# Optimization experiments

Hardware: AMD Instinct MI355X
Metric: run time of the kernel (lower is better)

The kernel has to match this reference:

```python
import jax, jax.numpy as jnp
import numpy as np

B, T, S, D, H, DK = 2, 2048, 2048, 1024, 16, 64


def setup_inputs() -> dict:
    key = jax.random.key(0)
    ks = jax.random.split(key, 11)
    s = 1.0 / np.sqrt(D)
    return {
        "query": jax.random.normal(ks[0], (B, T, D), jnp.float32),
        "value": jax.random.normal(ks[1], (B, S, D), jnp.float32),
        "key": jax.random.normal(ks[2], (B, S, D), jnp.float32),
        "Wq": jax.random.normal(ks[3], (D, H, DK), jnp.float32) * s,
        "bq": jnp.zeros((H, DK), jnp.float32),
        "Wk": jax.random.normal(ks[4], (D, H, DK), jnp.float32) * s,
        "bk": jnp.zeros((H, DK), jnp.float32),
        "Wv": jax.random.normal(ks[5], (D, H, DK), jnp.float32) * s,
        "bv": jnp.zeros((H, DK), jnp.float32),
        "Wo": jax.random.normal(ks[6], (H, DK, D), jnp.float32) * (1.0 / np.sqrt(H * DK)),
        "bo": jnp.zeros((D,), jnp.float32),
    }


def reference(query, value, key, Wq, bq, Wk, bk, Wv, bv, Wo, bo):
    # Projections: (B, seq, D) x (D, H, DK) -> (B, seq, H, DK)
    q = jnp.einsum("btd,dhk->bthk", query, Wq) + bq
    k = jnp.einsum("bsd,dhk->bshk", key, Wk) + bk
    v = jnp.einsum("bsd,dhk->bshk", value, Wv) + bv
    # Scaled dot-product attention (keras scales query by 1/sqrt(key_dim))
    q = q * (1.0 / np.sqrt(DK)).astype(np.float32)
    scores = jnp.einsum("bshk,bthk->bhts", k, q)  # (B, H, T, S)
    probs = jax.nn.softmax(scores, axis=-1)
    attn = jnp.einsum("bhts,bshk->bthk", probs, v)  # (B, T, H, DK)
    # Output projection back to model dim
    out = jnp.einsum("bthk,hkd->btd", attn, Wo) + bo
    return out
```

## Files before the change

### kernel.cpp

```cpp
#include <hip/hip_runtime.h>
#include <math.h>

#define BB  2
#define TT  2048
#define SSQ 2048
#define DD  1024
#define HH  16
#define DKK 64
#define MM  (BB*TT)
#define NN  (HH*DKK)

typedef __attribute__((ext_vector_type(8))) short short8;
typedef __attribute__((ext_vector_type(4))) float f32x4;
typedef __attribute__((ext_vector_type(2))) unsigned int uint2v;
typedef __attribute__((ext_vector_type(4))) unsigned int u32x4;

__device__ __forceinline__ short f2bf(float x) {
    unsigned u = __builtin_bit_cast(unsigned, x);
    unsigned r = (u + 0x7FFFu + ((u >> 16) & 1u)) >> 16;
    return (short)r;
}

__device__ __forceinline__ unsigned pk2(float lo, float hi) {
    return (__builtin_bit_cast(unsigned, hi) & 0xFFFF0000u) |
           (__builtin_bit_cast(unsigned, lo) >> 16);
}

__device__ __forceinline__ void glds16(const void* g, void* l) {
    __builtin_amdgcn_global_load_lds(
        (const __attribute__((address_space(1))) void*)g,
        (__attribute__((address_space(3))) void*)l, 16, 0, 0);
}

__global__ __launch_bounds__(256)
void to_bf16_acts(const float* __restrict__ a0, const float* __restrict__ a1,
                  const float* __restrict__ a2,
                  short* __restrict__ o0, short* __restrict__ o1,
                  short* __restrict__ o2)
{
    int z = blockIdx.y;
    const float* in = (z == 0) ? a0 : (z == 1) ? a1 : a2;
    short* out = (z == 0) ? o0 : (z == 1) ? o1 : o2;
    size_t i0 = ((size_t)blockIdx.x * 256 + threadIdx.x) * 8;
    f32x4 f0 = *(const f32x4*)(in + i0);
    f32x4 f1 = *(const f32x4*)(in + i0 + 4);
    short8 v;
#pragma unroll
    for (int j = 0; j < 4; j++) v[j] = f2bf(f0[j]);
#pragma unroll
    for (int j = 0; j < 4; j++) v[4 + j] = f2bf(f1[j]);
    *(short8*)(out + i0) = v;
}

__global__ __launch_bounds__(256)
void wtrans(const float* __restrict__ w0, const float* __restrict__ w1,
            const float* __restrict__ w2, const float* __restrict__ w3,
            short* __restrict__ t0, short* __restrict__ t1,
            short* __restrict__ t2, short* __restrict__ t3)
{
    __shared__ float Ls[64][65];
    int z = blockIdx.z;
    const float* in = (z == 0) ? w0 : (z == 1) ? w1 : (z == 2) ? w2 : w3;
    short* out = (z == 0) ? t0 : (z == 1) ? t1 : (z == 2) ? t2 : t3;
    const int r0 = blockIdx.y * 64, c0 = blockIdx.x * 64;
    const int t = threadIdx.x;
    const int r = t >> 2, c4 = t & 3;

    const float* src = in + (size_t)(r0 + r) * DD + c0 + c4 * 16;
#pragma unroll
    for (int i = 0; i < 4; i++) {
        f32x4 f = *(const f32x4*)(src + i * 4);
#pragma unroll
        for (int j = 0; j < 4; j++) Ls[r][c4 * 16 + i * 4 + j] = f[j];
    }
    __syncthreads();

    short8 va, vb;
#pragma unroll
    for (int j = 0; j < 8; j++) va[j] = f2bf(Ls[c4 * 16 + j][r]);
#pragma unroll
    for (int j = 0; j < 8; j++) vb[j] = f2bf(Ls[c4 * 16 + 8 + j][r]);
    short* dst = out + (size_t)(c0 + r) * DD + r0 + c4 * 16;
    *(short8*)dst = va;
    *(short8*)(dst + 8) = vb;
}

__global__ __launch_bounds__(256, 3)
void gemm_qkv(const short* __restrict__ Aq, const short* __restrict__ Ak,
              const short* __restrict__ Av,
              const short* __restrict__ Wqt, const short* __restrict__ Wkt,
              const short* __restrict__ Wvt,
              const float* __restrict__ bq, const float* __restrict__ bk,
              const float* __restrict__ bv,
              short* __restrict__ Qb, short* __restrict__ Kb,
              short* __restrict__ Vbt)
{
    __shared__ short As[2][128 * 32];
    __shared__ short Bs[2][128 * 32];

    const int d = blockIdx.x + 8 * blockIdx.y + 256 * blockIdx.z;
    const int kx = d & 7, j = d >> 3;
    const int z = j >> 5;
    const int n0 = ((j >> 2) & 7) * 128;
    const int m0 = (4 * kx + (j & 3)) * 128;

    const short* A  = (z == 0) ? Aq : (z == 1) ? Ak : Av;
    const short* Bt = (z == 0) ? Wqt : (z == 1) ? Wkt : Wvt;
    const float* bias = (z == 0) ? bq : (z == 1) ? bk : bv;

    const int tid = threadIdx.x;
    const int w = tid >> 6, l = tid & 63;
    const int l15 = l & 15, quad = l >> 4;
    const int wm = w >> 1, wn = w & 1;
    const int r = tid >> 2, cseg = tid & 3;

    f32x4 acc[4][4];
#pragma unroll
    for (int i = 0; i < 4; i++)
#pragma unroll
        for (int jj = 0; jj < 4; jj++) acc[i][jj] = (f32x4){0.f, 0.f, 0.f, 0.f};

    const short* gA = A + (size_t)(m0 + r) * DD + cseg * 8;
    const short* gB = Bt + (size_t)(n0 + r) * DD + cseg * 8;

    glds16(gA + 0,               &As[0][w * 512]);
    glds16(gA + (size_t)64 * DD, &As[0][2048 + w * 512]);
    glds16(gB + 0,               &Bs[0][w * 512]);
    glds16(gB + (size_t)64 * DD, &Bs[0][2048 + w * 512]);

    for (int k0 = 0; k0 < DD; k0 += 32) {
        const int cur = (k0 >> 5) & 1;
        __syncthreads();
        if (k0 + 32 < DD) {
            glds16(gA + k0 + 32,                   &As[cur ^ 1][w * 512]);
            glds16(gA + (size_t)64 * DD + k0 + 32, &As[cur ^ 1][2048 + w * 512]);
            glds16(gB + k0 + 32,                   &Bs[cur ^ 1][w * 512]);
            glds16(gB + (size_t)64 * DD + k0 + 32, &Bs[cur ^ 1][2048 + w * 512]);
        }

        short8 bF[4];
#pragma unroll
        for (int ni = 0; ni < 4; ni++)
            bF[ni] = *(const short8*)&Bs[cur][(wn * 64 + ni * 16 + l15) * 32 + quad * 8];
        if (z != 2) {
#pragma unroll
            for (int mi = 0; mi < 4; mi++) {
                short8 aF = *(const short8*)&As[cur][(wm * 64 + mi * 16 + l15) * 32 + quad * 8];
#pragma unroll
                for (int ni = 0; ni < 4; ni++)
                    acc[mi][ni] = __builtin_amdgcn_mfma_f32_16x16x32_bf16(aF, bF[ni], acc[mi][ni], 0, 0, 0);
            }
        } else {
#pragma unroll
            for (int mi = 0; mi < 4; mi++) {
                short8 aF = *(const short8*)&As[cur][(wm * 64 + mi * 16 + l15) * 32 + quad * 8];
#pragma unroll
                for (int ni = 0; ni < 4; ni++)
                    acc[ni][mi] = __builtin_amdgcn_mfma_f32_16x16x32_bf16(bF[ni], aF, acc[ni][mi], 0, 0, 0);
            }
        }
    }

    if (z != 2) {
        short* dst = (z == 0) ? Qb : Kb;
        const float scale = (z == 0) ? 0.1803368801f : 1.0f;
#pragma unroll
        for (int mi = 0; mi < 4; mi++) {
#pragma unroll
            for (int reg = 0; reg < 4; reg++) {
                int m = m0 + wm * 64 + mi * 16 + quad * 4 + reg;
                int b = m >> 11, t = m & 2047;
#pragma unroll
                for (int ni = 0; ni < 4; ni++) {
                    int n = n0 + wn * 64 + ni * 16 + l15;
                    float vv = (acc[mi][ni][reg] + bias[n]) * scale;
                    int h = n >> 6, dk = n & 63;
                    dst[((size_t)(b * HH + h) * TT + t) * DKK + dk] = f2bf(vv);
                }
            }
        }
    } else {
        const int b = m0 >> 11;
        const int tl0 = (m0 & 2047) + wm * 64;
#pragma unroll
        for (int ni = 0; ni < 4; ni++) {
#pragma unroll
            for (int reg = 0; reg < 4; reg++) {
                int n = n0 + wn * 64 + ni * 16 + quad * 4 + reg;
                int h = n >> 6, dk = n & 63;
                float bb = bias[n];
                short* vrow = Vbt + ((size_t)(b * HH + h) * DKK + dk) * SSQ;
#pragma unroll
                for (int mi = 0; mi < 4; mi++) {
                    int t = tl0 + mi * 16 + l15;
                    vrow[t] = f2bf(acc[ni][mi][reg] + bb);
                }
            }
        }
    }
}

__global__ __launch_bounds__(256, 3)
void gemm_out(const short* __restrict__ Ab, const short* __restrict__ Wot,
              const float* __restrict__ bo, float* __restrict__ out)
{
    __shared__ short As[2][2 * 64 * 32];
    __shared__ short Bs[2][2 * 128 * 32];

    const int d = blockIdx.x + 8 * blockIdx.y;
    const int kx = d & 7, j = d >> 3;
    const int m0 = (8 * kx + (j & 7)) * 64;
    const int n0 = (j >> 3) * 128;

    const int tid = threadIdx.x;
    const int w = tid >> 6, l = tid & 63;
    const int l15 = l & 15, quad = l >> 4;
    const int wm = w >> 1, wn = w & 1;

    f32x4 acc[2][4];
#pragma unroll
    for (int i = 0; i < 2; i++)
#pragma unroll
        for (int jj = 0; jj < 4; jj++) acc[i][jj] = (f32x4){0.f, 0.f, 0.f, 0.f};

    const int r = tid >> 2, cseg = tid & 3;
    const short* gA = Ab + (size_t)(m0 + r) * DD + cseg * 8;
    const short* gB = Wot + (size_t)(n0 + r) * DD + cseg * 8;

#define STAGE_OUT(buf, k0)                                                     \
    do {                                                                       \
        glds16(gA + (k0),                        &As[buf][w * 512]);           \
        glds16(gA + (k0) + 32,                   &As[buf][2048 + w * 512]);    \
        glds16(gB + (k0),                        &Bs[buf][w * 512]);           \
        glds16(gB + (size_t)64 * DD + (k0),      &Bs[buf][2048 + w * 512]);    \
        glds16(gB + (k0) + 32,                   &Bs[buf][4096 + w * 512]);    \
        glds16(gB + (size_t)64 * DD + (k0) + 32, &Bs[buf][6144 + w * 512]);    \
    } while (0)

    STAGE_OUT(0, 0);

    for (int k0 = 0; k0 < DD; k0 += 64) {
        const int cur = (k0 >> 6) & 1;
        __syncthreads();
        if (k0 + 64 < DD) STAGE_OUT(cur ^ 1, k0 + 64);

#pragma unroll
        for (int kk = 0; kk < 2; kk++) {
            short8 bF[4];
#pragma unroll
            for (int ni = 0; ni < 4; ni++)
                bF[ni] = *(const short8*)&Bs[cur][kk * 4096 + (wn * 64 + ni * 16 + l15) * 32 + quad * 8];
#pragma unroll
            for (int mi = 0; mi < 2; mi++) {
                short8 aF = *(const short8*)&As[cur][kk * 2048 + (wm * 32 + mi * 16 + l15) * 32 + quad * 8];
#pragma unroll
                for (int ni = 0; ni < 4; ni++)
                    acc[mi][ni] = __builtin_amdgcn_mfma_f32_16x16x32_bf16(aF, bF[ni], acc[mi][ni], 0, 0, 0);
            }
        }
    }
#undef STAGE_OUT

#pragma unroll
    for (int mi = 0; mi < 2; mi++) {
#pragma unroll
        for (int reg = 0; reg < 4; reg++) {
            int m = m0 + wm * 32 + mi * 16 + quad * 4 + reg;
#pragma unroll
            for (int ni = 0; ni < 4; ni++) {
                int n = n0 + wn * 64 + ni * 16 + l15;
                out[(size_t)m * DD + n] = acc[mi][ni][reg] + bo[n];
            }
        }
    }
}

__global__ __launch_bounds__(256, 4)
void attn_mfma(const short* __restrict__ Qb, const short* __restrict__ Kb,
               const short* __restrict__ Vbt,
               float* __restrict__ O1, float* __restrict__ O2,
               float* __restrict__ l1, float* __restrict__ l2)
{
    __shared__ short KV[2 * 2 * 64 * 72];

    const int tid = threadIdx.x;
    const int w = tid >> 6, l = tid & 63;
    const int l15 = l & 15, quad = l >> 4;

    const int fid = blockIdx.y * 16 + blockIdx.x;
    const int swz = (fid & 7) * 64 + (fid >> 3);
    const int t0 = (swz & 15) * 128;
    const int bh = swz >> 4;
    const int half = blockIdx.z;
    const size_t hb = (size_t)bh * SSQ * DKK;
    const int r = tid >> 2, c4 = tid & 3;
    const int sbase = half * 1024;

    short8 qf[2][2];
#pragma unroll
    for (int mf = 0; mf < 2; mf++)
#pragma unroll
        for (int kk = 0; kk < 2; kk++)
            qf[mf][kk] = *(const short8*)(Qb + hb +
                (size_t)(t0 + 32 * w + 16 * mf + l15) * DKK + kk * 32 + quad * 8);

    const short* gkb = Kb + hb + (size_t)(sbase + r) * DKK + c4 * 16;
    const short* gvb = Vbt + hb + (size_t)r * SSQ + sbase + c4 * 16;
    short8 kr0 = *(const short8*)(gkb + 0);
    short8 kr1 = *(const short8*)(gkb + 8);
    short8 vr0 = *(const short8*)(gvb + 0);
    short8 vr1 = *(const short8*)(gvb + 8);

    f32x4 o[2][4];
#pragma unroll
    for (int mf = 0; mf < 2; mf++)
#pragma unroll
        for (int j = 0; j < 4; j++) o[mf][j] = (f32x4){0.f, 0.f, 0.f, 0.f};
    f32x4 lacc[2] = {(f32x4){0.f, 0.f, 0.f, 0.f}, (f32x4){0.f, 0.f, 0.f, 0.f}};
    const short8 ones = {(short)0x3F80, (short)0x3F80, (short)0x3F80, (short)0x3F80,
                         (short)0x3F80, (short)0x3F80, (short)0x3F80, (short)0x3F80};

    short* skb = KV + r * 72 + c4 * 16;

    for (int s0 = 0; s0 < 1024; s0 += 64) {
        const int dbo = (s0 & 64) ? 9216 : 0;
        *(short8*)(skb + dbo)          = kr0;
        *(short8*)(skb + dbo + 8)      = kr1;
        *(short8*)(skb + dbo + 4608)   = vr0;
        *(short8*)(skb + dbo + 4616)   = vr1;
        if (s0 + 64 < 1024) {
            const short* gk = gkb + (size_t)(s0 + 64) * DKK;
            const short* gv = gvb + (s0 + 64);
            kr0 = *(const short8*)(gk + 0);
            kr1 = *(const short8*)(gk + 8);
            vr0 = *(const short8*)(gv + 0);
            vr1 = *(const short8*)(gv + 8);
        }
        __syncthreads();
        const short* kb_ = KV + dbo;
        const short* vb_ = kb_ + 4608;

        f32x4 sc[4][2];
#pragma unroll
        for (int np = 0; np < 4; np++)
#pragma unroll
            for (int mf = 0; mf < 2; mf++) sc[np][mf] = (f32x4){0.f, 0.f, 0.f, 0.f};
        __builtin_amdgcn_s_setprio(1);
#pragma unroll
        for (int kk = 0; kk < 2; kk++) {
#pragma unroll
            for (int np = 0; np < 4; np++) {
                short8 aK = *(const short8*)&kb_[(16 * np + l15) * 72 + kk * 32 + quad * 8];
                sc[np][0] = __builtin_amdgcn_mfma_f32_16x16x32_bf16(aK, qf[0][kk], sc[np][0], 0, 0, 0);
                sc[np][1] = __builtin_amdgcn_mfma_f32_16x16x32_bf16(aK, qf[1][kk], sc[np][1], 0, 0, 0);
            }
        }
        __builtin_amdgcn_s_setprio(0);

        short8 pa[2][2];
#pragma unroll
        for (int mf = 0; mf < 2; mf++) {
#pragma unroll
            for (int kk = 0; kk < 2; kk++) {
                u32x4 wd;
#pragma unroll
                for (int b = 0; b < 2; b++) {
                    float p00 = __builtin_amdgcn_exp2f(sc[2 * kk][mf][2 * b]);
                    float p01 = __builtin_amdgcn_exp2f(sc[2 * kk][mf][2 * b + 1]);
                    float p10 = __builtin_amdgcn_exp2f(sc[2 * kk + 1][mf][2 * b]);
                    float p11 = __builtin_amdgcn_exp2f(sc[2 * kk + 1][mf][2 * b + 1]);
                    unsigned Xw = pk2(p00, p01);
                    unsigned Yw = pk2(p10, p11);
                    uint2v s1 = __builtin_amdgcn_permlane32_swap(Xw, Yw, false, false);
                    uint2v s2 = __builtin_amdgcn_permlane16_swap(s1[0], s1[1], false, false);
                    wd[b]     = s2[0];
                    wd[2 + b] = s2[1];
                }
                pa[mf][kk] = __builtin_bit_cast(short8, wd);
            }
        }

        __builtin_amdgcn_s_setprio(1);
#pragma unroll
        for (int kk = 0; kk < 2; kk++) {
            lacc[0] = __builtin_amdgcn_mfma_f32_16x16x32_bf16(pa[0][kk], ones, lacc[0], 0, 0, 0);
            lacc[1] = __builtin_amdgcn_mfma_f32_16x16x32_bf16(pa[1][kk], ones, lacc[1], 0, 0, 0);
#pragma unroll
            for (int np = 0; np < 4; np++) {
                short8 bV = *(const short8*)&vb_[(16 * np + l15) * 72 + kk * 32 + quad * 8];
                o[0][np] = __builtin_amdgcn_mfma_f32_16x16x32_bf16(pa[0][kk], bV, o[0][np], 0, 0, 0);
                o[1][np] = __builtin_amdgcn_mfma_f32_16x16x32_bf16(pa[1][kk], bV, o[1][np], 0, 0, 0);
            }
        }
        __builtin_amdgcn_s_setprio(0);
    }

    float* O = half ? O2 : O1;
    float* L = half ? l2 : l1;
    const size_t rowb = (size_t)bh * TT;
#pragma unroll
    for (int mf = 0; mf < 2; mf++) {
#pragma unroll
        for (int reg = 0; reg < 4; reg++) {
            int t = t0 + 32 * w + 16 * mf + quad * 4 + reg;
            if (l15 == 0) L[rowb + t] = lacc[mf][reg];
            float* orow = O + (rowb + t) * DKK;
#pragma unroll
            for (int np = 0; np < 4; np++)
                orow[16 * np + l15] = o[mf][np][reg];
        }
    }
}

__global__ __launch_bounds__(256)
void combine_norm(const float* __restrict__ O1, const float* __restrict__ O2,
                  const float* __restrict__ l1, const float* __restrict__ l2,
                  short* __restrict__ Ab)
{
    size_t g = (size_t)blockIdx.x * 256 + threadIdx.x;
    size_t i0 = g * 8;
    int bh = (int)(i0 >> 17);
    int t  = (int)((i0 >> 6) & 2047);
    int dk = (int)(i0 & 63);
    float inv = 1.f / (l1[(size_t)bh * TT + t] + l2[(size_t)bh * TT + t]);
    f32x4 a0 = *(const f32x4*)(O1 + i0);
    f32x4 a1 = *(const f32x4*)(O1 + i0 + 4);
    f32x4 b0 = *(const f32x4*)(O2 + i0);
    f32x4 b1 = *(const f32x4*)(O2 + i0 + 4);
    short8 v;
#pragma unroll
    for (int j = 0; j < 4; j++) v[j] = f2bf((a0[j] + b0[j]) * inv);
#pragma unroll
    for (int j = 0; j < 4; j++) v[4 + j] = f2bf((a1[j] + b1[j]) * inv);
    int b = bh >> 4, h = bh & 15;
    *(short8*)(Ab + (((size_t)(b * TT + t) * HH + h) * DKK + dk)) = v;
}

extern "C" void kernel_launch(void* const* d_in, const int* in_sizes, int n_in,
                              void* d_out, int out_size, void* d_ws, size_t ws_size,
                              hipStream_t stream)
{
    const float* query = (const float*)d_in[0];
    const float* value = (const float*)d_in[1];
    const float* key   = (const float*)d_in[2];
    const float* Wq    = (const float*)d_in[3];
    const float* bq    = (const float*)d_in[4];
    const float* Wk    = (const float*)d_in[5];
    const float* bk    = (const float*)d_in[6];
    const float* Wv    = (const float*)d_in[7];
    const float* bv    = (const float*)d_in[8];
    const float* Wo    = (const float*)d_in[9];
    const float* bo    = (const float*)d_in[10];
    float* out = (float*)d_out;

    const size_t actE = (size_t)MM * DD;
    const size_t wE   = (size_t)DD * NN;
    short* p = (short*)d_ws;
    short* Aq   = p; p += actE;
    short* Ak   = p; p += actE;
    short* Av   = p; p += actE;
    short* Wqt  = p; p += wE;
    short* Wkt  = p; p += wE;
    short* Wvt  = p; p += wE;
    short* Wot  = p; p += wE;
    short* Qb   = p; p += actE;
    short* Kb   = p; p += actE;
    short* Vbt  = p; p += actE;
    short* Ab   = p; p += actE;
    float* O2f  = (float*)p; p += 2 * actE;
    float* O1f  = (float*)Aq;
    float* l1f  = (float*)Av;
    float* l2f  = l1f + (size_t)BB * HH * TT;

    dim3 blk(256);

    to_bf16_acts<<<dim3((unsigned)(actE / 2048), 3), blk, 0, stream>>>(
        query, key, value, Aq, Ak, Av);

    wtrans<<<dim3(16, 16, 4), blk, 0, stream>>>(Wq, Wk, Wv, Wo, Wqt, Wkt, Wvt, Wot);

    gemm_qkv<<<dim3(NN / 128, MM / 128, 3), blk, 0, stream>>>(
        Aq, Ak, Av, Wqt, Wkt, Wvt, bq, bk, bv, Qb, Kb, Vbt);

    attn_mfma<<<dim3(TT / 128, BB * HH, 2), blk, 0, stream>>>(
        Qb, Kb, Vbt, O1f, O2f, l1f, l2f);

    combine_norm<<<dim3((unsigned)(actE / 2048)), blk, 0, stream>>>(
        O1f, O2f, l1f, l2f, Ab);

    gemm_out<<<dim3(NN / 128, MM / 64), blk, 0, stream>>>(Ab, Wot, bo, out);
}
```

Baseline: 225.4 us.

## Drop split-S attention and fuse normalization; merge prep kernels into one launch

The attention kernel no longer splits the key sequence into two halves written as fp32 partials. Each block now loops over all of S and writes normalized bf16 output straight into the head-interleaved layout, so the combine_norm kernel and its fp32 round trip go away. The activation cast and weight transpose kernels are merged into a single prep launch, and attention launch bounds drop from 4 to 3 waves. The trade-off is half as many attention blocks (512 instead of 1024) with twice the serial length each, which may reduce occupancy and latency hiding.

```diff
diff --git a/kernel.cpp b/kernel.cpp
--- a/kernel.cpp
+++ b/kernel.cpp
@@ -33,56 +33,60 @@
 }
 
 __global__ __launch_bounds__(256)
-void to_bf16_acts(const float* __restrict__ a0, const float* __restrict__ a1,
-                  const float* __restrict__ a2,
-                  short* __restrict__ o0, short* __restrict__ o1,
-                  short* __restrict__ o2)
-{
-    int z = blockIdx.y;
-    const float* in = (z == 0) ? a0 : (z == 1) ? a1 : a2;
-    short* out = (z == 0) ? o0 : (z == 1) ? o1 : o2;
-    size_t i0 = ((size_t)blockIdx.x * 256 + threadIdx.x) * 8;
-    f32x4 f0 = *(const f32x4*)(in + i0);
-    f32x4 f1 = *(const f32x4*)(in + i0 + 4);
-    short8 v;
-#pragma unroll
-    for (int j = 0; j < 4; j++) v[j] = f2bf(f0[j]);
-#pragma unroll
-    for (int j = 0; j < 4; j++) v[4 + j] = f2bf(f1[j]);
-    *(short8*)(out + i0) = v;
-}
-
-__global__ __launch_bounds__(256)
-void wtrans(const float* __restrict__ w0, const float* __restrict__ w1,
-            const float* __restrict__ w2, const float* __restrict__ w3,
-            short* __restrict__ t0, short* __restrict__ t1,
-            short* __restrict__ t2, short* __restrict__ t3)
+void prep(const float* __restrict__ aq, const float* __restrict__ ak,
+          const float* __restrict__ av,
+          const float* __restrict__ w0, const float* __restrict__ w1,
+          const float* __restrict__ w2, const float* __restrict__ w3,
+          short* __restrict__ oq, short* __restrict__ ok,
+          short* __restrict__ ov,
+          short* __restrict__ t0, short* __restrict__ t1,
+          short* __restrict__ t2, short* __restrict__ t3)
 {
     __shared__ float Ls[64][65];
-    int z = blockIdx.z;
-    const float* in = (z == 0) ? w0 : (z == 1) ? w1 : (z == 2) ? w2 : w3;
-    short* out = (z == 0) ? t0 : (z == 1) ? t1 : (z == 2) ? t2 : t3;
-    const int r0 = blockIdx.y * 64, c0 = blockIdx.x * 64;
-    const int t = threadIdx.x;
-    const int r = t >> 2, c4 = t & 3;
-
-    const float* src = in + (size_t)(r0 + r) * DD + c0 + c4 * 16;
-#pragma unroll
-    for (int i = 0; i < 4; i++) {
-        f32x4 f = *(const f32x4*)(src + i * 4);
-#pragma unroll
-        for (int j = 0; j < 4; j++) Ls[r][c4 * 16 + i * 4 + j] = f[j];
-    }
-    __syncthreads();
-
-    short8 va, vb;
-#pragma unroll
-    for (int j = 0; j < 8; j++) va[j] = f2bf(Ls[c4 * 16 + j][r]);
-#pragma unroll
-    for (int j = 0; j < 8; j++) vb[j] = f2bf(Ls[c4 * 16 + 8 + j][r]);
-    short* dst = out + (size_t)(c0 + r) * DD + r0 + c4 * 16;
-    *(short8*)dst = va;
-    *(short8*)(dst + 8) = vb;
+    const int id = blockIdx.x;
+    const int tid = threadIdx.x;
+
+    if (id < 6144) {
+        const int z = id >> 11;
+        const int x = id & 2047;
+        const float* in = (z == 0) ? aq : (z == 1) ? ak : av;
+        short* out = (z == 0) ? oq : (z == 1) ? ok : ov;
+        size_t i0 = ((size_t)x * 256 + tid) * 8;
+        f32x4 f0 = *(const f32x4*)(in + i0);
+        f32x4 f1 = *(const f32x4*)(in + i0 + 4);
+        short8 v;
+#pragma unroll
+        for (int j = 0; j < 4; j++) v[j] = f2bf(f0[j]);
+#pragma unroll
+        for (int j = 0; j < 4; j++) v[4 + j] = f2bf(f1[j]);
+        *(short8*)(out + i0) = v;
+    } else {
+        const int wid = id - 6144;
+        const int z = wid >> 8;
+        const int rem = wid & 255;
+        const float* in = (z == 0) ? w0 : (z == 1) ? w1 : (z == 2) ? w2 : w3;
+        short* out = (z == 0) ? t0 : (z == 1) ? t1 : (z == 2) ? t2 : t3;
+        const int c0 = (rem & 15) * 64, r0 = (rem >> 4) * 64;
+        const int r = tid >> 2, c4 = tid & 3;
+
+        const float* src = in + (size_t)(r0 + r) * DD + c0 + c4 * 16;
+#pragma unroll
+        for (int i = 0; i < 4; i++) {
+            f32x4 f = *(const f32x4*)(src + i * 4);
+#pragma unroll
+            for (int j = 0; j < 4; j++) Ls[r][c4 * 16 + i * 4 + j] = f[j];
+        }
+        __syncthreads();
+
+        short8 va, vb;
+#pragma unroll
+        for (int j = 0; j < 8; j++) va[j] = f2bf(Ls[c4 * 16 + j][r]);
+#pragma unroll
+        for (int j = 0; j < 8; j++) vb[j] = f2bf(Ls[c4 * 16 + 8 + j][r]);
+        short* dst = out + (size_t)(c0 + r) * DD + r0 + c4 * 16;
+        *(short8*)dst = va;
+        *(short8*)(dst + 8) = vb;
+    }
 }
 
 __global__ __launch_bounds__(256, 3)
@@ -275,11 +279,9 @@
     }
 }
 
-__global__ __launch_bounds__(256, 4)
+__global__ __launch_bounds__(256, 3)
 void attn_mfma(const short* __restrict__ Qb, const short* __restrict__ Kb,
-               const short* __restrict__ Vbt,
-               float* __restrict__ O1, float* __restrict__ O2,
-               float* __restrict__ l1, float* __restrict__ l2)
+               const short* __restrict__ Vbt, short* __restrict__ Ab)
 {
     __shared__ short KV[2 * 2 * 64 * 72];
 
@@ -291,10 +293,8 @@
     const int swz = (fid & 7) * 64 + (fid >> 3);
     const int t0 = (swz & 15) * 128;
     const int bh = swz >> 4;
-    const int half = blockIdx.z;
     const size_t hb = (size_t)bh * SSQ * DKK;
     const int r = tid >> 2, c4 = tid & 3;
-    const int sbase = half * 1024;
 
     short8 qf[2][2];
 #pragma unroll
@@ -304,8 +304,8 @@
             qf[mf][kk] = *(const short8*)(Qb + hb +
                 (size_t)(t0 + 32 * w + 16 * mf + l15) * DKK + kk * 32 + quad * 8);
 
-    const short* gkb = Kb + hb + (size_t)(sbase + r) * DKK + c4 * 16;
-    const short* gvb = Vbt + hb + (size_t)r * SSQ + sbase + c4 * 16;
+    const short* gkb = Kb + hb + (size_t)r * DKK + c4 * 16;
+    const short* gvb = Vbt + hb + (size_t)r * SSQ + c4 * 16;
     short8 kr0 = *(const short8*)(gkb + 0);
     short8 kr1 = *(const short8*)(gkb + 8);
     short8 vr0 = *(const short8*)(gvb + 0);
@@ -322,13 +322,13 @@
 
     short* skb = KV + r * 72 + c4 * 16;
 
-    for (int s0 = 0; s0 < 1024; s0 += 64) {
+    for (int s0 = 0; s0 < SSQ; s0 += 64) {
         const int dbo = (s0 & 64) ? 9216 : 0;
         *(short8*)(skb + dbo)          = kr0;
         *(short8*)(skb + dbo + 8)      = kr1;
         *(short8*)(skb + dbo + 4608)   = vr0;
         *(short8*)(skb + dbo + 4616)   = vr1;
-        if (s0 + 64 < 1024) {
+        if (s0 + 64 < SSQ) {
             const short* gk = gkb + (size_t)(s0 + 64) * DKK;
             const short* gv = gvb + (s0 + 64);
             kr0 = *(const short8*)(gk + 0);
@@ -395,45 +395,20 @@
         __builtin_amdgcn_s_setprio(0);
     }
 
-    float* O = half ? O2 : O1;
-    float* L = half ? l2 : l1;
-    const size_t rowb = (size_t)bh * TT;
+    const int b = bh >> 4, h = bh & 15;
 #pragma unroll
     for (int mf = 0; mf < 2; mf++) {
 #pragma unroll
         for (int reg = 0; reg < 4; reg++) {
+            float inv = 1.f / lacc[mf][reg];
             int t = t0 + 32 * w + 16 * mf + quad * 4 + reg;
-            if (l15 == 0) L[rowb + t] = lacc[mf][reg];
-            float* orow = O + (rowb + t) * DKK;
-#pragma unroll
-            for (int np = 0; np < 4; np++)
-                orow[16 * np + l15] = o[mf][np][reg];
-        }
-    }
-}
-
-__global__ __launch_bounds__(256)
-void combine_norm(const float* __restrict__ O1, const float* __restrict__ O2,
-                  const float* __restrict__ l1, const float* __restrict__ l2,
-                  short* __restrict__ Ab)
-{
-    size_t g = (size_t)blockIdx.x * 256 + threadIdx.x;
-    size_t i0 = g * 8;
-    int bh = (int)(i0 >> 17);
-    int t  = (int)((i0 >> 6) & 2047);
-    int dk = (int)(i0 & 63);
-    float inv = 1.f / (l1[(size_t)bh * TT + t] + l2[(size_t)bh * TT + t]);
-    f32x4 a0 = *(const f32x4*)(O1 + i0);
-    f32x4 a1 = *(const f32x4*)(O1 + i0 + 4);
-    f32x4 b0 = *(const f32x4*)(O2 + i0);
-    f32x4 b1 = *(const f32x4*)(O2 + i0 + 4);
-    short8 v;
-#pragma unroll
-    for (int j = 0; j < 4; j++) v[j] = f2bf((a0[j] + b0[j]) * inv);
-#pragma unroll
-    for (int j = 0; j < 4; j++) v[4 + j] = f2bf((a1[j] + b1[j]) * inv);
-    int b = bh >> 4, h = bh & 15;
-    *(short8*)(Ab + (((size_t)(b * TT + t) * HH + h) * DKK + dk)) = v;
+#pragma unroll
+            for (int np = 0; np < 4; np++) {
+                Ab[((size_t)(b * TT + t) * HH + h) * DKK + 16 * np + l15] =
+                    f2bf(o[mf][np][reg] * inv);
+            }
+        }
+    }
 }
 
 extern "C" void kernel_launch(void* const* d_in, const int* in_sizes, int n_in,
@@ -467,26 +442,16 @@
     short* Kb   = p; p += actE;
     short* Vbt  = p; p += actE;
     short* Ab   = p; p += actE;
-    float* O2f  = (float*)p; p += 2 * actE;
-    float* O1f  = (float*)Aq;
-    float* l1f  = (float*)Av;
-    float* l2f  = l1f + (size_t)BB * HH * TT;
 
     dim3 blk(256);
 
-    to_bf16_acts<<<dim3((unsigned)(actE / 2048), 3), blk, 0, stream>>>(
-        query, key, value, Aq, Ak, Av);
-
-    wtrans<<<dim3(16, 16, 4), blk, 0, stream>>>(Wq, Wk, Wv, Wo, Wqt, Wkt, Wvt, Wot);
+    prep<<<dim3(7168), blk, 0, stream>>>(
+        query, key, value, Wq, Wk, Wv, Wo, Aq, Ak, Av, Wqt, Wkt, Wvt, Wot);
 
     gemm_qkv<<<dim3(NN / 128, MM / 128, 3), blk, 0, stream>>>(
         Aq, Ak, Av, Wqt, Wkt, Wvt, bq, bk, bv, Qb, Kb, Vbt);
 
-    attn_mfma<<<dim3(TT / 128, BB * HH, 2), blk, 0, stream>>>(
-        Qb, Kb, Vbt, O1f, O2f, l1f, l2f);
-
-    combine_norm<<<dim3((unsigned)(actE / 2048)), blk, 0, stream>>>(
-        O1f, O2f, l1f, l2f, Ab);
+    attn_mfma<<<dim3(TT / 128, BB * HH), blk, 0, stream>>>(Qb, Kb, Vbt, Ab);
 
     gemm_out<<<dim3(NN / 128, MM / 64), blk, 0, stream>>>(Ab, Wot, bo, out);
 }
```

After: 217.2 us. -3.6%, faster.
